# Optimization experiments

Hardware: AMD Instinct MI355X
Metric: run time of the kernel (lower is better)

The kernel has to match this reference:

```python
import jax, jax.numpy as jnp
import numpy as np

HAND_EDGES = [(0,1),(1,2),(2,3),(3,4),(0,5),(5,6),(6,7),(7,8),(0,9),(9,10),(10,11),(11,12),(0,13),(13,14),(14,15),(15,16),(0,17),(17,18),(18,19),(19,20),(5,9),(9,13),(13,17)]
N_JOINTS = 21
B = 16384
IN_DIM = 256
OUT_DIM = 64  # head_dim of MultiHeadGraphAttention(256, 256, num_heads=4)


def build_hand_adjacency_matrix():
    adj = np.zeros((N_JOINTS, N_JOINTS), dtype=np.float32)
    for i, j in HAND_EDGES:
        adj[i, j] = 1.0
        adj[j, i] = 1.0
    adj = adj + np.eye(N_JOINTS, dtype=np.float32)
    deg = np.clip(adj.sum(axis=1, keepdims=True), 1.0, None)
    adj = adj / np.sqrt(deg) / np.sqrt(deg).T
    return jnp.asarray(adj)


def setup_inputs() -> dict:
    key = jax.random.key(0)
    k1, k2, k3 = jax.random.split(key, 3)
    h = jax.random.normal(k1, (B, N_JOINTS, IN_DIM), dtype=jnp.float32)
    W = jax.random.normal(k2, (IN_DIM, OUT_DIM), dtype=jnp.float32) * (IN_DIM ** -0.5)
    a = jax.random.normal(k3, (2 * OUT_DIM,), dtype=jnp.float32) * ((2 * OUT_DIM) ** -0.5)
    adj = build_hand_adjacency_matrix()
    return {"h": h, "adj": adj, "W": W, "a": a}


def reference(h, adj, W, a):
    # h: [B, N, in_dim], adj: [N, N], W: [in_dim, out_dim], a: [2*out_dim]
    Wh = jnp.einsum('bni,io->bno', h, W)              # [B, N, out_dim]
    # a @ concat(Wh_i, Wh_j) == (Wh_i @ a_src) + (Wh_j @ a_dst); avoids [B,N,N,2D]
    a_src, a_dst = a[:OUT_DIM], a[OUT_DIM:]
    s_src = Wh @ a_src                                # [B, N]
    s_dst = Wh @ a_dst                                # [B, N]
    e = s_src[:, :, None] + s_dst[:, None, :]         # [B, N, N]
    e = jnp.where(e >= 0, e, 0.2 * e)                 # LeakyReLU(0.2)
    e = jnp.where((adj == 0)[None, :, :], -jnp.inf, e)
    alpha = jax.nn.softmax(e, axis=-1)                # [B, N, N]
    return jnp.einsum('bnm,bmo->bno', alpha, Wh)      # [B, N, out_dim]
```

## Files before the change

### kernel.cpp

```cpp
#include <hip/hip_runtime.h>

#define NB 16384
#define NJ 21
#define KD 256
#define OD 64
#define NT 5
#define MROWS (NB * NJ)
#define MT (MROWS / 16)
#define NBLKA 768
#define NWA (NBLKA * 4)
#define NBLKB 2048
#define NWB (NBLKB * 4)
#define STS 68

#define WS_SC    40960
#define WS_WH    (40960 + 2752512)

typedef __attribute__((ext_vector_type(8))) short short8;
typedef __attribute__((ext_vector_type(4))) float f32x4;

__constant__ int c_nbr[NJ][6] = {
  {0,1,5,9,13,17},{0,1,2,0,0,0},{1,2,3,0,0,0},{2,3,4,0,0,0},{3,4,0,0,0,0},
  {0,5,6,9,0,0},{5,6,7,0,0,0},{6,7,8,0,0,0},{7,8,0,0,0,0},
  {0,5,9,10,13,0},{9,10,11,0,0,0},{10,11,12,0,0,0},{11,12,0,0,0,0},
  {0,9,13,14,17,0},{13,14,15,0,0,0},{14,15,16,0,0,0},{15,16,0,0,0,0},
  {0,13,17,18,0,0},{17,18,19,0,0,0},{18,19,20,0,0,0},{19,20,0,0,0,0}
};
__constant__ int c_deg[NJ] = {6,3,3,3,2,4,3,3,2,5,3,3,2,5,3,3,2,4,3,3,2};

constexpr int OE_CNT[NJ] = {6,3,3,3,2,4,3,3,2,5,3,3,2,5,3,3,2,4,3,3,2};
constexpr int OE_N[NJ][6] = {
  {0,1,5,9,13,17},{0,1,2,0,0,0},{1,2,3,0,0,0},{2,3,4,0,0,0},{3,4,0,0,0,0},
  {0,5,6,9,0,0},{5,6,7,0,0,0},{6,7,8,0,0,0},{7,8,0,0,0,0},
  {0,5,9,10,13,0},{9,10,11,0,0,0},{10,11,12,0,0,0},{11,12,0,0,0,0},
  {0,9,13,14,17,0},{13,14,15,0,0,0},{14,15,16,0,0,0},{15,16,0,0,0,0},
  {0,13,17,18,0,0},{17,18,19,0,0,0},{18,19,20,0,0,0},{19,20,0,0,0,0}
};
constexpr int OE_J[NJ][6] = {
  {0,0,0,0,0,0},{1,1,0,0,0,0},{2,1,0,0,0,0},{2,1,0,0,0,0},{2,1,0,0,0,0},
  {2,1,0,1,0,0},{2,1,0,0,0,0},{2,1,0,0,0,0},{2,1,0,0,0,0},
  {3,3,2,0,1,0},{3,1,0,0,0,0},{2,1,0,0,0,0},{2,1,0,0,0,0},
  {4,4,2,0,1,0},{3,1,0,0,0,0},{2,1,0,0,0,0},{2,1,0,0,0,0},
  {5,4,2,0,0,0},{3,1,0,0,0,0},{2,1,0,0,0,0},{2,1,0,0,0,0}
};

__device__ inline unsigned int f2bf(float f) {
  unsigned int u = __float_as_uint(f);
  u += 0x7FFFu + ((u >> 16) & 1u);
  return u >> 16;
}

__device__ __forceinline__ short8 mk8(float4 lo, float4 hi) {
  union { unsigned int u[4]; short8 s; } r;
  r.u[0] = f2bf(lo.x) | (f2bf(lo.y) << 16);
  r.u[1] = f2bf(lo.z) | (f2bf(lo.w) << 16);
  r.u[2] = f2bf(hi.x) | (f2bf(hi.y) << 16);
  r.u[3] = f2bf(hi.z) | (f2bf(hi.w) << 16);
  return r.s;
}

__global__ __launch_bounds__(256)
void pack_w(const float* __restrict__ W, const float* __restrict__ a,
            unsigned short* __restrict__ ws) {
  __shared__ float va[KD], vd[KD];
  const int t = threadIdx.x;
  {
    const float* Wr = W + t * OD;
    float s0 = 0.f, s1 = 0.f;
    #pragma unroll 8
    for (int o = 0; o < OD; ++o) { s0 = fmaf(Wr[o], a[o], s0); s1 = fmaf(Wr[o], a[OD + o], s1); }
    va[t] = s0; vd[t] = s1;
  }
  __syncthreads();
  for (int e = t; e < 8 * NT * 64; e += 256) {
    const int f = e >> 6, ll = e & 63;
    const int ks = f / NT, nt = f - ks * NT;
    const int col = nt * 16 + (ll & 15);
    const int qq = ll >> 4;
    unsigned short v[8];
    #pragma unroll
    for (int j = 0; j < 8; ++j) {
      const int k = ks * 32 + ((j >> 2) << 4) + qq * 4 + (j & 3);
      float x;
      if (col < OD)            x = W[k * OD + col];
      else if (col == OD)      x = va[k];
      else if (col == OD + 1)  x = vd[k];
      else                     x = 0.f;
      v[j] = (unsigned short)f2bf(x);
    }
    #pragma unroll
    for (int j = 0; j < 8; ++j) ws[e * 8 + j] = v[j];
  }
}

__global__ __launch_bounds__(256, 3)
void gemm_a(const float* __restrict__ h, const uint4* __restrict__ bfrag,
            unsigned short* __restrict__ wh, float* __restrict__ sc) {
  __shared__ short8 Bl[8 * NT * 64];
  __shared__ __align__(16) unsigned short st_[4][16 * STS];
  __shared__ float ss_[4][32];

  const int t = threadIdx.x;
  const int wv = t >> 6, l = t & 63, q = l >> 4, c = l & 15;
  unsigned short* st = st_[wv];
  float* ssst = ss_[wv];

  {
    uint4* dst = (uint4*)Bl;
    #pragma unroll
    for (int i = 0; i < 10; ++i) dst[t + i * 256] = bfrag[t + i * 256];
  }
  __syncthreads();

  const int gw = blockIdx.x * 4 + wv;
  const float4* hb4 = (const float4*)h;
  const size_t lofs = (size_t)c * 64 + q;

  const float4* Ar = hb4 + (size_t)gw * 1024 + lofs;
  float4 L[4], H[4];
  #pragma unroll
  for (int p = 0; p < 4; ++p) { L[p] = Ar[p * 8]; H[p] = Ar[p * 8 + 4]; }

  for (int mt = gw; mt < MT; mt += NWA) {
    const int mtn = (mt + NWA < MT) ? (mt + NWA) : mt;
    const float4* Arn = hb4 + (size_t)mtn * 1024 + lofs;
    const int R = mt * 16;

    f32x4 acc[NT];
    #pragma unroll
    for (int nt = 0; nt < NT; ++nt) acc[nt] = (f32x4){0.f, 0.f, 0.f, 0.f};

    #pragma unroll
    for (int ks = 0; ks < 8; ++ks) {
      const int s = ks & 3;
      const float4 lo = L[s], hi = H[s];
      if (ks < 4) { L[s] = Ar[(ks + 4) * 8];  H[s] = Ar[(ks + 4) * 8 + 4]; }
      else        { L[s] = Arn[(ks - 4) * 8]; H[s] = Arn[(ks - 4) * 8 + 4]; }
      const short8 A = mk8(lo, hi);
      #pragma unroll
      for (int nt = 0; nt < NT; ++nt)
        acc[nt] = __builtin_amdgcn_mfma_f32_16x16x32_bf16(A, Bl[(ks * NT + nt) * 64 + l],
                                                          acc[nt], 0, 0, 0);
    }

    #pragma unroll
    for (int nt = 0; nt < 4; ++nt)
      #pragma unroll
      for (int r = 0; r < 4; ++r)
        st[(q * 4 + r) * STS + nt * 16 + c] = (unsigned short)f2bf(acc[nt][r]);
    if (c < 2) {
      #pragma unroll
      for (int r = 0; r < 4; ++r) ssst[(q * 4 + r) * 2 + c] = acc[4][r];
    }
    __builtin_amdgcn_sched_barrier(0);

    {
      const int row = l >> 3;
      const int cs  = (l & 7) * 8;
      uint4 v0 = *(const uint4*)(st + row * STS + cs);
      uint4 v1 = *(const uint4*)(st + (row + 8) * STS + cs);
      uint4* dst = (uint4*)(wh + (size_t)R * OD);
      dst[l] = v0;
      dst[64 + l] = v1;
      if (l < 32) sc[(size_t)R * 2 + l] = ssst[l];
    }
    __builtin_amdgcn_sched_barrier(0);
    Ar = Arn;
  }
}

__global__ __launch_bounds__(256)
void epi_b(const unsigned short* __restrict__ wh, const float* __restrict__ sc,
           float* __restrict__ out) {
  __shared__ __align__(16) unsigned short Wl_[4][NJ * OD + 16];
  __shared__ float aL_[4][NJ * 8];
  const int t = threadIdx.x, wv = t >> 6, l = t & 63;
  unsigned short* Wl = Wl_[wv];
  float* aL = aL_[wv];

  const int gw = blockIdx.x * 4 + wv;
  for (int b = gw; b < NB; b += NWB) {
    const uint4* src = (const uint4*)(wh + (size_t)b * NJ * OD);
    uint4* dst = (uint4*)Wl;
    dst[l] = src[l];
    dst[64 + l] = src[64 + l];
    if (l < 40) dst[128 + l] = src[128 + l];

    const int ln = (l < NJ) ? l : 0;
    const float2 s2 = ((const float2*)sc)[(size_t)b * NJ + ln];
    const float ss = s2.x, sd = s2.y;

    float sdm[6];
    #pragma unroll
    for (int j = 0; j < 6; ++j) sdm[j] = __shfl(sd, c_nbr[ln][j]);

    if (l < NJ) {
      const int deg = c_deg[l];
      float e[6]; float mx = -1e30f;
      #pragma unroll
      for (int j = 0; j < 6; ++j) {
        float ev = ss + sdm[j];
        ev = (ev >= 0.f) ? ev : 0.2f * ev;
        e[j] = (j < deg) ? ev : -1e30f;
        mx = fmaxf(mx, e[j]);
      }
      float ex[6]; float sum = 0.f;
      #pragma unroll
      for (int j = 0; j < 6; ++j) { ex[j] = __expf(e[j] - mx); sum += ex[j]; }
      const float inv = 1.f / sum;
      #pragma unroll
      for (int j = 0; j < 6; ++j) aL[l * 8 + j] = ex[j] * inv;
    }
    asm volatile("s_waitcnt lgkmcnt(0)" ::: "memory");
    __builtin_amdgcn_sched_barrier(0);

    float acc[NJ];
    #pragma unroll
    for (int n = 0; n < NJ; ++n) acc[n] = 0.f;
    #pragma unroll
    for (int m = 0; m < NJ; ++m) {
      const float w = __uint_as_float(((unsigned int)Wl[m * OD + l]) << 16);
      #pragma unroll
      for (int i = 0; i < 6; ++i) {
        if (i < OE_CNT[m]) {
          const int n = OE_N[m][i];
          acc[n] = fmaf(aL[n * 8 + OE_J[m][i]], w, acc[n]);
        }
      }
    }
    float* ob = out + (size_t)b * NJ * OD;
    #pragma unroll
    for (int n = 0; n < NJ; ++n) ob[n * OD + l] = acc[n];

    asm volatile("s_waitcnt lgkmcnt(0)" ::: "memory");
    __builtin_amdgcn_sched_barrier(0);
  }
}

extern "C" void kernel_launch(void* const* d_in, const int* in_sizes, int n_in,
                              void* d_out, int out_size, void* d_ws, size_t ws_size,
                              hipStream_t stream) {
  (void)in_sizes; (void)n_in; (void)out_size; (void)ws_size;
  const float* h = (const float*)d_in[0];
  const float* W = (const float*)d_in[2];
  const float* a = (const float*)d_in[3];
  float* out = (float*)d_out;

  unsigned short* ws = (unsigned short*)d_ws;
  unsigned short* wh = (unsigned short*)((char*)d_ws + WS_WH);
  float* sc = (float*)((char*)d_ws + WS_SC);

  hipLaunchKernelGGL(pack_w, dim3(1), dim3(256), 0, stream, W, a, ws);
  hipLaunchKernelGGL(gemm_a, dim3(NBLKA), dim3(256), 0, stream,
                     h, (const uint4*)ws, wh, sc);
  hipLaunchKernelGGL(epi_b, dim3(NBLKB), dim3(256), 0, stream,
                     (const unsigned short*)wh, (const float*)sc, out);
}
```

Measured before the change: 122.7 us.

## Coalesce h loads via swizzled LDS staging; stream B fragments from global

The GEMM kernel now loads each 16-row tile of h with fully coalesced contiguous float4 reads (one row-chunk per lane), converts to bf16, and writes into a per-wave XOR-swizzled LDS buffer from which MFMA A operands are read. Before, each lane read strided pieces directly. B fragments are no longer staged in shared memory but double-buffered in registers from global/L2 each k-step, and pack_w is spread over 20 blocks. This trades the strided global access pattern for extra LDS traffic and register pressure (16 float4 prefetch registers plus B buffers), which may reduce occupancy under the 3-block launch bound.

```diff
diff --git a/kernel.cpp b/kernel.cpp
--- a/kernel.cpp
+++ b/kernel.cpp
@@ -17,6 +17,7 @@
 #define WS_WH    (40960 + 2752512)
 
 typedef __attribute__((ext_vector_type(8))) short short8;
+typedef __attribute__((ext_vector_type(4))) short s16x4;
 typedef __attribute__((ext_vector_type(4))) float f32x4;
 
 __constant__ int c_nbr[NJ][6] = {
@@ -50,15 +51,6 @@
   return u >> 16;
 }
 
-__device__ __forceinline__ short8 mk8(float4 lo, float4 hi) {
-  union { unsigned int u[4]; short8 s; } r;
-  r.u[0] = f2bf(lo.x) | (f2bf(lo.y) << 16);
-  r.u[1] = f2bf(lo.z) | (f2bf(lo.w) << 16);
-  r.u[2] = f2bf(hi.x) | (f2bf(hi.y) << 16);
-  r.u[3] = f2bf(hi.z) | (f2bf(hi.w) << 16);
-  return r.s;
-}
-
 __global__ __launch_bounds__(256)
 void pack_w(const float* __restrict__ W, const float* __restrict__ a,
             unsigned short* __restrict__ ws) {
@@ -72,7 +64,7 @@
     va[t] = s0; vd[t] = s1;
   }
   __syncthreads();
-  for (int e = t; e < 8 * NT * 64; e += 256) {
+  for (int e = blockIdx.x * 256 + t; e < 8 * NT * 64; e += gridDim.x * 256) {
     const int f = e >> 6, ll = e & 63;
     const int ks = f / NT, nt = f - ks * NT;
     const int col = nt * 16 + (ll & 15);
@@ -94,53 +86,71 @@
 }
 
 __global__ __launch_bounds__(256, 3)
-void gemm_a(const float* __restrict__ h, const uint4* __restrict__ bfrag,
+void gemm_a(const float* __restrict__ h, const short8* __restrict__ bfr,
             unsigned short* __restrict__ wh, float* __restrict__ sc) {
-  __shared__ short8 Bl[8 * NT * 64];
+  __shared__ __align__(16) char At_[4][8192];
   __shared__ __align__(16) unsigned short st_[4][16 * STS];
   __shared__ float ss_[4][32];
 
   const int t = threadIdx.x;
   const int wv = t >> 6, l = t & 63, q = l >> 4, c = l & 15;
+  char* At = At_[wv];
   unsigned short* st = st_[wv];
   float* ssst = ss_[wv];
 
+  const float4* hb4 = (const float4*)h;
+  const int gw = blockIdx.x * 4 + wv;
+  const int sw = (c & 7) << 4;
+
+  float4 G[16];
   {
-    uint4* dst = (uint4*)Bl;
-    #pragma unroll
-    for (int i = 0; i < 10; ++i) dst[t + i * 256] = bfrag[t + i * 256];
-  }
-  __syncthreads();
-
-  const int gw = blockIdx.x * 4 + wv;
-  const float4* hb4 = (const float4*)h;
-  const size_t lofs = (size_t)c * 64 + q;
-
-  const float4* Ar = hb4 + (size_t)gw * 1024 + lofs;
-  float4 L[4], H[4];
-  #pragma unroll
-  for (int p = 0; p < 4; ++p) { L[p] = Ar[p * 8]; H[p] = Ar[p * 8 + 4]; }
+    const float4* tb = hb4 + (size_t)gw * 1024 + l;
+    #pragma unroll
+    for (int r = 0; r < 16; ++r) G[r] = tb[r * 64];
+  }
 
   for (int mt = gw; mt < MT; mt += NWA) {
-    const int mtn = (mt + NWA < MT) ? (mt + NWA) : mt;
-    const float4* Arn = hb4 + (size_t)mtn * 1024 + lofs;
     const int R = mt * 16;
+    const int mtn = mt + NWA;
+    const bool haveNext = (mtn < MT);
+
+    #pragma unroll
+    for (int r = 0; r < 16; ++r) {
+      uint2 pk;
+      pk.x = f2bf(G[r].x) | (f2bf(G[r].y) << 16);
+      pk.y = f2bf(G[r].z) | (f2bf(G[r].w) << 16);
+      *(uint2*)(At + ((r * 512 + l * 8) ^ ((r & 7) << 4))) = pk;
+    }
+
+    if (haveNext) {
+      const float4* tbn = hb4 + (size_t)mtn * 1024 + l;
+      #pragma unroll
+      for (int r = 0; r < 16; ++r) G[r] = tbn[r * 64];
+    }
 
     f32x4 acc[NT];
     #pragma unroll
     for (int nt = 0; nt < NT; ++nt) acc[nt] = (f32x4){0.f, 0.f, 0.f, 0.f};
 
+    short8 Bf[2][NT];
+    #pragma unroll
+    for (int nt = 0; nt < NT; ++nt) Bf[0][nt] = bfr[nt * 64 + l];
+
     #pragma unroll
     for (int ks = 0; ks < 8; ++ks) {
-      const int s = ks & 3;
-      const float4 lo = L[s], hi = H[s];
-      if (ks < 4) { L[s] = Ar[(ks + 4) * 8];  H[s] = Ar[(ks + 4) * 8 + 4]; }
-      else        { L[s] = Arn[(ks - 4) * 8]; H[s] = Arn[(ks - 4) * 8 + 4]; }
-      const short8 A = mk8(lo, hi);
+      const int cur = ks & 1;
+      if (ks < 7) {
+        #pragma unroll
+        for (int nt = 0; nt < NT; ++nt)
+          Bf[cur ^ 1][nt] = bfr[((ks + 1) * NT + nt) * 64 + l];
+      }
+      const int ba = c * 512 + ks * 64 + q * 8;
+      s16x4 alo = *(const s16x4*)(At + (ba ^ sw));
+      s16x4 ahi = *(const s16x4*)(At + ((ba + 32) ^ sw));
+      short8 A = __builtin_shufflevector(alo, ahi, 0, 1, 2, 3, 4, 5, 6, 7);
       #pragma unroll
       for (int nt = 0; nt < NT; ++nt)
-        acc[nt] = __builtin_amdgcn_mfma_f32_16x16x32_bf16(A, Bl[(ks * NT + nt) * 64 + l],
-                                                          acc[nt], 0, 0, 0);
+        acc[nt] = __builtin_amdgcn_mfma_f32_16x16x32_bf16(A, Bf[cur][nt], acc[nt], 0, 0, 0);
     }
 
     #pragma unroll
@@ -165,7 +175,6 @@
       if (l < 32) sc[(size_t)R * 2 + l] = ssst[l];
     }
     __builtin_amdgcn_sched_barrier(0);
-    Ar = Arn;
   }
 }
 
@@ -250,9 +259,9 @@
   unsigned short* wh = (unsigned short*)((char*)d_ws + WS_WH);
   float* sc = (float*)((char*)d_ws + WS_SC);
 
-  hipLaunchKernelGGL(pack_w, dim3(1), dim3(256), 0, stream, W, a, ws);
+  hipLaunchKernelGGL(pack_w, dim3(20), dim3(256), 0, stream, W, a, ws);
   hipLaunchKernelGGL(gemm_a, dim3(NBLKA), dim3(256), 0, stream,
-                     h, (const uint4*)ws, wh, sc);
+                     h, (const short8*)ws, wh, sc);
   hipLaunchKernelGGL(epi_b, dim3(NBLKB), dim3(256), 0, stream,
                      (const unsigned short*)wh, (const float*)sc, out);
 }
```

Result: slower. 219.2 us (+78.7%).
